# Kernel optimization log

Measured on AMD Instinct MI355X. Metric: run time of the kernel, lower is better.

The kernel has to match this reference:

```python
import jax, jax.numpy as jnp
import numpy as np

D_MODEL = 512
N_HEADS = 8
D_FF = 2048
B, L = 4, 2048
EPS = 1e-5


def _layernorm(x, g, b):
    mu = jnp.mean(x, axis=-1, keepdims=True)
    var = jnp.mean(jnp.square(x - mu), axis=-1, keepdims=True)
    return (x - mu) * jax.lax.rsqrt(var + EPS) * g + b


def setup_inputs() -> dict:
    key = jax.random.key(0)
    ks = jax.random.split(key, 8)
    s = 0.02
    return {
        'x': jax.random.normal(ks[0], (B, L, D_MODEL), jnp.float32),
        'Wq': jax.random.normal(ks[1], (D_MODEL, D_MODEL), jnp.float32) * s,
        'bq': jnp.zeros((D_MODEL,), jnp.float32),
        'Wk': jax.random.normal(ks[2], (D_MODEL, D_MODEL), jnp.float32) * s,
        'bk': jnp.zeros((D_MODEL,), jnp.float32),
        'Wv': jax.random.normal(ks[3], (D_MODEL, D_MODEL), jnp.float32) * s,
        'bv': jnp.zeros((D_MODEL,), jnp.float32),
        'Wo': jax.random.normal(ks[4], (D_MODEL, D_MODEL), jnp.float32) * s,
        'bo': jnp.zeros((D_MODEL,), jnp.float32),
        'W1': jax.random.normal(ks[5], (D_MODEL, D_FF), jnp.float32) * s,
        'b1': jnp.zeros((D_FF,), jnp.float32),
        'W2': jax.random.normal(ks[6], (D_FF, D_MODEL), jnp.float32) * s,
        'b2': jnp.zeros((D_MODEL,), jnp.float32),
        'g1': jnp.ones((D_MODEL,), jnp.float32),
        'be1': jnp.zeros((D_MODEL,), jnp.float32),
        'g2': jnp.ones((D_MODEL,), jnp.float32),
        'be2': jnp.zeros((D_MODEL,), jnp.float32),
    }


def reference(x, Wq, bq, Wk, bk, Wv, bv, Wo, bo, W1, b1, W2, b2, g1, be1, g2, be2):
    B_, L_, D = x.shape
    H = N_HEADS
    E = D // H
    q = (x @ Wq + bq).reshape(B_, L_, H, E)
    k = (x @ Wk + bk).reshape(B_, L_, H, E)
    v = (x @ Wv + bv).reshape(B_, L_, H, E)
    scale = 1.0 / jnp.sqrt(jnp.float32(E))
    # full [B,H,L,S] scores (mask_flag=False -> no causal mask)
    scores = jnp.einsum('blhe,bshe->bhls', q, k)
    A = jax.nn.softmax(scale * scores, axis=-1)
    V = jnp.einsum('bhls,bshd->blhd', A, v).reshape(B_, L_, D)
    attn_out = V @ Wo + bo
    x = _layernorm(x + attn_out, g1, be1)
    h = jax.nn.gelu(x @ W1 + b1, approximate=False)  # torch nn.GELU default = exact erf
    x = _layernorm(x + (h @ W2 + b2), g2, be2)
    return x
```

## Files before the change

### kernel.cpp

```cpp
#include <hip/hip_runtime.h>
#include <math.h>

#define DM 512
#define LSEQ 2048
#define BATCH 4
#define NH 8
#define EH 64
#define DFF 2048
#define MTOK (BATCH*LSEQ)
#define QKVW 1536
#define QSCL 0.18033688011112042f

using short8  = __attribute__((ext_vector_type(8))) short;
using floatx4 = __attribute__((ext_vector_type(4))) float;

__device__ __forceinline__ short f2b(float f) {
    unsigned u = __float_as_uint(f);
    return (short)((u + 0x7FFFu + ((u >> 16) & 1u)) >> 16);
}
__device__ __forceinline__ float b2f(short s) {
    return __uint_as_float(((unsigned)(unsigned short)s) << 16);
}
__device__ __forceinline__ void load_lds16(const short* g, short* l) {
    __builtin_amdgcn_global_load_lds(
        (const __attribute__((address_space(1))) void*)g,
        (__attribute__((address_space(3))) void*)l, 16, 0, 0);
}
#define MFMA_BF16(a, b, c) __builtin_amdgcn_mfma_f32_16x16x32_bf16(a, b, c, 0, 0, 0)

__global__ __launch_bounds__(256) void prep_kernel(
    const float* __restrict__ Wq, const float* __restrict__ Wk,
    const float* __restrict__ Wv, const float* __restrict__ Wo,
    const float* __restrict__ W1, const float* __restrict__ W2,
    const float* __restrict__ x,
    const float* __restrict__ bq, const float* __restrict__ bk,
    const float* __restrict__ bv,
    short* __restrict__ Wqkvt, short* __restrict__ Wot,
    short* __restrict__ W1t, short* __restrict__ W2t,
    short* __restrict__ xb, float* __restrict__ bqkv)
{
    __shared__ float t[64][65];
    const int bid = blockIdx.x;
    const int tid = threadIdx.x;

    if (bid >= 2880) {
        #pragma unroll
        for (int j = 0; j < 6; ++j) {
            const int i = j * 256 + tid;
            bqkv[i] = (i < 512) ? bq[i] : (i < 1024 ? bk[i - 512] : bv[i - 1024]);
        }
        return;
    }
    if (bid >= 832) {
        const long i = ((long)(bid - 832) * 256 + tid) * 8;
        float4 a = *(const float4*)(x + i);
        float4 b = *(const float4*)(x + i + 4);
        short tt[8] = { f2b(a.x), f2b(a.y), f2b(a.z), f2b(a.w),
                        f2b(b.x), f2b(b.y), f2b(b.z), f2b(b.w) };
        *(float4*)(xb + i) = *(float4*)tt;
        return;
    }
    const float* src; short* dst; int C, R, bx, by;
    if (bid < 256) {
        const int w = bid >> 6, sub = bid & 63;
        src = (w == 0) ? Wq : (w == 1) ? Wk : Wv;
        dst = Wqkvt + (long)w * 262144;
        R = 512; C = 512; bx = sub & 7; by = sub >> 3;
    } else if (bid < 320) {
        const int sub = bid - 256;
        src = Wo; dst = Wot; R = 512; C = 512; bx = sub & 7; by = sub >> 3;
    } else if (bid < 576) {
        const int sub = bid - 320;
        src = W1; dst = W1t; R = 512; C = 2048; bx = sub & 31; by = sub >> 5;
    } else {
        const int sub = bid - 576;
        src = W2; dst = W2t; R = 2048; C = 512; bx = sub & 7; by = sub >> 3;
    }
    const int r0 = by * 64, c0 = bx * 64;
    const int r = tid >> 2, cs = (tid & 3) * 16;
    const float* ip = src + (long)(r0 + r) * C + c0 + cs;
    #pragma unroll
    for (int i = 0; i < 4; ++i) {
        float4 v = *(const float4*)(ip + i * 4);
        t[r][cs + i*4 + 0] = v.x; t[r][cs + i*4 + 1] = v.y;
        t[r][cs + i*4 + 2] = v.z; t[r][cs + i*4 + 3] = v.w;
    }
    __syncthreads();
    short tmp[16];
    #pragma unroll
    for (int j = 0; j < 16; ++j) tmp[j] = f2b(t[cs + j][r]);
    short* op = dst + (long)(c0 + r) * R + r0 + cs;
    *(float4*)op       = *(float4*)&tmp[0];
    *(float4*)(op + 8) = *(float4*)&tmp[8];
}

template<int TN, int DO_GELU, int QKV>
__global__ __launch_bounds__(256, 4) void mfma_gemm(
    const short* __restrict__ A, const short* __restrict__ Bt,
    const float* __restrict__ bias, short* __restrict__ C,
    short* __restrict__ VtOut, int M, int N, int K, int lda, int ldc)
{
    constexpr int NJ = TN / 32;
    constexpr int NB = TN / 64;
    __shared__ short As[2][128][32];
    __shared__ short Bs[2][TN][32];

    const int tid  = threadIdx.x;
    const int wave = tid >> 6;
    const int lane = tid & 63;
    const int qd   = lane >> 4;
    const int sl   = lane & 15;
    const int m0 = blockIdx.y * 128;
    const int n0 = blockIdx.x * TN;
    const int wm = (wave & 1) * 64;
    const int wn = (wave >> 1) * (TN / 2);
    const int srow = lane >> 2;
    const int scol = (lane & 3) * 8;

    floatx4 acc[4][NJ];
    const floatx4 fz = {0.f, 0.f, 0.f, 0.f};
    #pragma unroll
    for (int i = 0; i < 4; ++i)
        #pragma unroll
        for (int j = 0; j < NJ; ++j) acc[i][j] = fz;

    const short* Abase = A  + (long)m0 * lda + scol;
    const short* Bbase = Bt + (long)n0 * K   + scol;

    #pragma unroll
    for (int it = 0; it < 2; ++it) {
        const int rg = wave * 2 + it;
        load_lds16(Abase + (long)(rg*16 + srow) * lda, &As[0][rg * 16][0]);
    }
    #pragma unroll
    for (int it = 0; it < NB; ++it) {
        const int rg = wave * NB + it;
        load_lds16(Bbase + (long)(rg*16 + srow) * K, &Bs[0][rg * 16][0]);
    }

    const int NIT = K / 32;
    for (int kit = 0; kit < NIT; ++kit) {
        const int cur = kit & 1;
        __syncthreads();
        if (kit + 1 < NIT) {
            const int nk = (kit + 1) * 32;
            #pragma unroll
            for (int it = 0; it < 2; ++it) {
                const int rg = wave * 2 + it;
                load_lds16(Abase + (long)(rg*16 + srow) * lda + nk, &As[1 - cur][rg * 16][0]);
            }
            #pragma unroll
            for (int it = 0; it < NB; ++it) {
                const int rg = wave * NB + it;
                load_lds16(Bbase + (long)(rg*16 + srow) * K + nk, &Bs[1 - cur][rg * 16][0]);
            }
        }
        short8 af[4], bf[NJ];
        #pragma unroll
        for (int t = 0; t < 4; ++t)
            af[t] = *(const short8*)&As[cur][wm + t*16 + sl][qd * 8];
        #pragma unroll
        for (int t = 0; t < NJ; ++t)
            bf[t] = *(const short8*)&Bs[cur][wn + t*16 + sl][qd * 8];
        #pragma unroll
        for (int i = 0; i < 4; ++i)
            #pragma unroll
            for (int j = 0; j < NJ; ++j)
                acc[i][j] = MFMA_BF16(af[i], bf[j], acc[i][j]);
    }

    #pragma unroll
    for (int j = 0; j < NJ; ++j) {
        const int col = n0 + wn + j*16 + sl;
        const float bv = bias[col];
        #pragma unroll
        for (int i = 0; i < 4; ++i) {
            #pragma unroll
            for (int r = 0; r < 4; ++r) {
                const int row = m0 + wm + i*16 + qd*4 + r;
                float v = acc[i][j][r] + bv;
                if (DO_GELU) v = 0.5f * v * (1.0f + erff(v * 0.70710678118654752f));
                if (QKV) {
                    if (col < 512) v *= QSCL;
                    const short bb = f2b(v);
                    if (col < 1024) {
                        C[(long)row * 1024 + col] = bb;
                    } else {
                        const int e = col - 1024;
                        const int b_ = row >> 11, l = row & 2047;
                        VtOut[(((long)(b_*8 + (e >> 6))) * 64 + (e & 63)) * 2048 + l] = bb;
                    }
                } else {
                    C[(long)row * ldc + col] = f2b(v);
                }
            }
        }
    }
}

__global__ __launch_bounds__(256, 3) void mfma_attn(
    const short* __restrict__ QK, const short* __restrict__ VtG,
    short* __restrict__ O)
{
    __shared__ short Ks[2][2][64][32];
    __shared__ short Vs[2][2][64][32];
    __shared__ short Ps[4][32][72];

    const int tid  = threadIdx.x;
    const int wave = tid >> 6;
    const int lane = tid & 63;
    const int qd   = lane >> 4;
    const int sl   = lane & 15;
    const int srow = lane >> 2;
    const int scol = (lane & 3) * 8;

    const int bid = blockIdx.x;
    const int h  = bid & 7;
    const int b  = (bid >> 3) & 3;
    const int qt = bid >> 5;
    const int tok0 = b * LSEQ;
    const int q0 = qt * 128;
    const short* Kbase = QK + (long)tok0 * 1024 + 512 + h * EH
                         + (long)(wave*16 + srow) * 1024 + scol;
    const short* Vbase = VtG + ((long)(b * NH + h)) * EH * 2048
                         + (long)(wave*16 + srow) * 2048 + scol;

    {
        const int lr = tid >> 1;
        const int lc = (tid & 1) * 32;
        const short* qp = QK + (long)(tok0 + q0 + lr) * 1024 + h * EH + lc;
        short* dp = &Ps[wave][lr & 31][lc];
        *(float4*)(dp)      = *(const float4*)(qp);
        *(float4*)(dp + 8)  = *(const float4*)(qp + 8);
        *(float4*)(dp + 16) = *(const float4*)(qp + 16);
        *(float4*)(dp + 24) = *(const float4*)(qp + 24);
    }
    short8 aq[2][2];
    #pragma unroll
    for (int q2 = 0; q2 < 2; ++q2)
        #pragma unroll
        for (int ks = 0; ks < 2; ++ks)
            aq[q2][ks] = *(const short8*)&Ps[wave][q2*16 + sl][ks*32 + qd*8];

    float l_i[2][4] = {};
    floatx4 oacc[2][4];
    const floatx4 fz = {0.f, 0.f, 0.f, 0.f};
    #pragma unroll
    for (int q2 = 0; q2 < 2; ++q2)
        #pragma unroll
        for (int t = 0; t < 4; ++t) oacc[q2][t] = fz;

    #pragma unroll
    for (int p = 0; p < 2; ++p) {
        load_lds16(Kbase + p*32,            &Ks[0][p][wave*16][0]);
        load_lds16(Vbase + p*32,            &Vs[0][p][wave*16][0]);
    }

    for (int kt = 0; kt < 32; ++kt) {
        const int cur = kt & 1;
        __syncthreads();
        if (kt + 1 < 32) {
            #pragma unroll
            for (int p = 0; p < 2; ++p) {
                load_lds16(Kbase + (long)(kt+1)*64*1024 + p*32, &Ks[1 - cur][p][wave*16][0]);
                load_lds16(Vbase + (kt+1)*64 + p*32,            &Vs[1 - cur][p][wave*16][0]);
            }
        }

        floatx4 s[2][4];
        #pragma unroll
        for (int q2 = 0; q2 < 2; ++q2)
            #pragma unroll
            for (int t = 0; t < 4; ++t) s[q2][t] = fz;
        #pragma unroll
        for (int ks = 0; ks < 2; ++ks)
            #pragma unroll
            for (int t = 0; t < 4; ++t) {
                short8 bk = *(const short8*)&Ks[cur][ks][t*16 + sl][qd * 8];
                s[0][t] = MFMA_BF16(aq[0][ks], bk, s[0][t]);
                s[1][t] = MFMA_BF16(aq[1][ks], bk, s[1][t]);
            }

        #pragma unroll
        for (int q2 = 0; q2 < 2; ++q2)
            #pragma unroll
            for (int t = 0; t < 4; ++t) {
                const int pg = (((t*2 + (sl >> 3)) ^ qd) << 3) | (sl & 7);
                #pragma unroll
                for (int r = 0; r < 4; ++r) {
                    const float pv = __builtin_amdgcn_exp2f(s[q2][t][r]);
                    l_i[q2][r] += pv;
                    Ps[wave][q2*16 + qd*4 + r][pg] = (short)(__float_as_uint(pv) >> 16);
                }
            }

        #pragma unroll
        for (int ks = 0; ks < 2; ++ks) {
            const int pgr = ((ks*4 + qd) ^ ((sl >> 2) & 3)) * 8;
            short8 ap0 = *(const short8*)&Ps[wave][sl][pgr];
            short8 ap1 = *(const short8*)&Ps[wave][16 + sl][pgr];
            #pragma unroll
            for (int t = 0; t < 4; ++t) {
                short8 bv = *(const short8*)&Vs[cur][ks][t*16 + sl][qd * 8];
                oacc[0][t] = MFMA_BF16(ap0, bv, oacc[0][t]);
                oacc[1][t] = MFMA_BF16(ap1, bv, oacc[1][t]);
            }
        }
    }

    float linv[2][4];
    #pragma unroll
    for (int q2 = 0; q2 < 2; ++q2)
        #pragma unroll
        for (int r = 0; r < 4; ++r) {
            float l = l_i[q2][r];
            l += __shfl_xor(l, 1);
            l += __shfl_xor(l, 2);
            l += __shfl_xor(l, 4);
            l += __shfl_xor(l, 8);
            linv[q2][r] = 1.0f / l;
        }
    #pragma unroll
    for (int q2 = 0; q2 < 2; ++q2)
        #pragma unroll
        for (int t = 0; t < 4; ++t)
            #pragma unroll
            for (int r = 0; r < 4; ++r) {
                const int row = tok0 + q0 + wave*32 + q2*16 + qd*4 + r;
                const int col = h * EH + t*16 + sl;
                O[(long)row * DM + col] = f2b(oacc[q2][t][r] * linv[q2][r]);
            }
}

template<int X_BF16, int OUT_F32>
__global__ __launch_bounds__(256) void add_ln_kernel(
    const void* __restrict__ Xv, const short* __restrict__ R,
    const float* __restrict__ g, const float* __restrict__ beta,
    void* __restrict__ outv)
{
    const int row = blockIdx.x;
    const int tid = threadIdx.x;
    float x0, x1;
    if (X_BF16) {
        const short* xp = (const short*)Xv + (long)row * DM;
        x0 = b2f(xp[tid]); x1 = b2f(xp[tid + 256]);
    } else {
        const float* xp = (const float*)Xv + (long)row * DM;
        x0 = xp[tid]; x1 = xp[tid + 256];
    }
    const short* rp = R + (long)row * DM;
    const float v0 = x0 + b2f(rp[tid]);
    const float v1 = x1 + b2f(rp[tid + 256]);
    float s = v0 + v1, sq = v0*v0 + v1*v1;
    #pragma unroll
    for (int o = 32; o > 0; o >>= 1) {
        s  += __shfl_down(s, o);
        sq += __shfl_down(sq, o);
    }
    __shared__ float ss[4], ssq[4];
    const int wid = tid >> 6, lane = tid & 63;
    if (lane == 0) { ss[wid] = s; ssq[wid] = sq; }
    __syncthreads();
    const float S  = ss[0] + ss[1] + ss[2] + ss[3];
    const float SQ = ssq[0] + ssq[1] + ssq[2] + ssq[3];
    const float mean = S * (1.0f / DM);
    const float var  = SQ * (1.0f / DM) - mean * mean;
    const float rstd = rsqrtf(var + 1e-5f);
    const float o0 = (v0 - mean) * rstd * g[tid] + beta[tid];
    const float o1 = (v1 - mean) * rstd * g[tid + 256] + beta[tid + 256];
    if (OUT_F32) {
        float* op = (float*)outv + (long)row * DM;
        op[tid] = o0; op[tid + 256] = o1;
    } else {
        short* op = (short*)outv + (long)row * DM;
        op[tid] = f2b(o0); op[tid + 256] = f2b(o1);
    }
}

extern "C" void kernel_launch(void* const* d_in, const int* in_sizes, int n_in,
                              void* d_out, int out_size, void* d_ws, size_t ws_size,
                              hipStream_t stream)
{
    const float* x   = (const float*)d_in[0];
    const float* Wq  = (const float*)d_in[1];
    const float* bq  = (const float*)d_in[2];
    const float* Wk  = (const float*)d_in[3];
    const float* bk  = (const float*)d_in[4];
    const float* Wv  = (const float*)d_in[5];
    const float* bv  = (const float*)d_in[6];
    const float* Wo  = (const float*)d_in[7];
    const float* bo  = (const float*)d_in[8];
    const float* W1  = (const float*)d_in[9];
    const float* b1  = (const float*)d_in[10];
    const float* W2  = (const float*)d_in[11];
    const float* b2  = (const float*)d_in[12];
    const float* g1  = (const float*)d_in[13];
    const float* be1 = (const float*)d_in[14];
    const float* g2  = (const float*)d_in[15];
    const float* be2 = (const float*)d_in[16];
    float* out = (float*)d_out;

    short* ws    = (short*)d_ws;
    short* Wqkvt = ws;
    short* Wot   = Wqkvt + 786432;
    short* W1t   = Wot + 262144;
    short* W2t   = W1t + 1048576;
    float* bqkv  = (float*)(W2t + 1048576);
    short* xb    = (short*)(bqkv + 1536);
    short* qk    = xb + 4194304;
    short* VtG   = qk + 8388608;
    short* Ob    = VtG + 4194304;
    short* res   = Ob + 4194304;
    short* hbuf  = qk;

    const dim3 blk(256);

    prep_kernel<<<dim3(2881), blk, 0, stream>>>(
        Wq, Wk, Wv, Wo, W1, W2, x, bq, bk, bv,
        Wqkvt, Wot, W1t, W2t, xb, bqkv);

    mfma_gemm<128, 0, 1><<<dim3(12, 64), blk, 0, stream>>>(
        xb, Wqkvt, bqkv, qk, VtG, MTOK, QKVW, DM, DM, 0);

    mfma_attn<<<dim3(512), blk, 0, stream>>>(qk, VtG, Ob);

    mfma_gemm<64, 0, 0><<<dim3(8, 64), blk, 0, stream>>>(
        Ob, Wot, bo, res, nullptr, MTOK, DM, DM, DM, DM);

    add_ln_kernel<0, 0><<<dim3(MTOK), blk, 0, stream>>>(x, res, g1, be1, xb);

    mfma_gemm<128, 1, 0><<<dim3(16, 64), blk, 0, stream>>>(
        xb, W1t, b1, hbuf, nullptr, MTOK, DFF, DM, DM, DFF);

    mfma_gemm<64, 0, 0><<<dim3(8, 64), blk, 0, stream>>>(
        hbuf, W2t, b2, res, nullptr, MTOK, DM, DFF, DFF, DM);

    add_ln_kernel<1, 1><<<dim3(MTOK), blk, 0, stream>>>(xb, res, g2, be2, out);
}
```

Measured before the change: 289.8 us.

## Halve attention query tile, compute transposed scores, use tanh GELU, vector V stores

The attention kernel now gives each wave 16 query rows instead of 32 and launches twice as many blocks. It computes S^T by swapping the MFMA operands so each lane packs four probabilities into one 8-byte LDS write, and the row sum is reduced with fewer shuffles. The GEMM epilogue swaps exact erf GELU for a tanh approximation built on exp2/rcp, and writes the transposed V output as packed 4-element stores using round-half-up bf16 packing. The intent is more parallelism and fewer scalar stores and transcendental ops, at the cost of reloading K/V tiles twice as often per query and a small deviation from exact GELU.

```diff
diff --git a/kernel.cpp b/kernel.cpp
--- a/kernel.cpp
+++ b/kernel.cpp
@@ -20,6 +20,17 @@
 }
 __device__ __forceinline__ float b2f(short s) {
     return __uint_as_float(((unsigned)(unsigned short)s) << 16);
+}
+__device__ __forceinline__ unsigned pack2bf(float lo, float hi) {
+    return __builtin_amdgcn_perm(__float_as_uint(hi) + 0x8000u,
+                                 __float_as_uint(lo) + 0x8000u, 0x07060302u);
+}
+__device__ __forceinline__ float gelu_tanh(float v) {
+    float v2 = v * v;
+    float y  = v * fmaf(0.0356774081f, v2, 0.7978845608f);
+    float e  = __builtin_amdgcn_exp2f(y * 2.885390082f);
+    float r  = __builtin_amdgcn_rcpf(e + 1.0f);
+    return v * (1.0f - r);
 }
 __device__ __forceinline__ void load_lds16(const short* g, short* l) {
     __builtin_amdgcn_global_load_lds(
@@ -172,27 +183,35 @@
     #pragma unroll
     for (int j = 0; j < NJ; ++j) {
         const int col = n0 + wn + j*16 + sl;
-        const float bv = bias[col];
+        const float bvs = bias[col];
         #pragma unroll
         for (int i = 0; i < 4; ++i) {
+            float v[4];
             #pragma unroll
             for (int r = 0; r < 4; ++r) {
-                const int row = m0 + wm + i*16 + qd*4 + r;
-                float v = acc[i][j][r] + bv;
-                if (DO_GELU) v = 0.5f * v * (1.0f + erff(v * 0.70710678118654752f));
-                if (QKV) {
-                    if (col < 512) v *= QSCL;
-                    const short bb = f2b(v);
-                    if (col < 1024) {
-                        C[(long)row * 1024 + col] = bb;
-                    } else {
-                        const int e = col - 1024;
-                        const int b_ = row >> 11, l = row & 2047;
-                        VtOut[(((long)(b_*8 + (e >> 6))) * 64 + (e & 63)) * 2048 + l] = bb;
-                    }
+                float tv = acc[i][j][r] + bvs;
+                if (DO_GELU) tv = gelu_tanh(tv);
+                v[r] = tv;
+            }
+            const int row0 = m0 + wm + i*16 + qd*4;
+            if (QKV) {
+                if (col < 1024) {
+                    const float s = (col < 512) ? QSCL : 1.0f;
+                    #pragma unroll
+                    for (int r = 0; r < 4; ++r)
+                        C[(long)(row0 + r) * 1024 + col] = f2b(v[r] * s);
                 } else {
-                    C[(long)row * ldc + col] = f2b(v);
+                    const int e = col - 1024;
+                    const int b_ = row0 >> 11, l0 = row0 & 2047;
+                    uint2 w;
+                    w.x = pack2bf(v[0], v[1]);
+                    w.y = pack2bf(v[2], v[3]);
+                    *(uint2*)&VtOut[(((long)(b_*8 + (e >> 6))) * 64 + (e & 63)) * 2048 + l0] = w;
                 }
+            } else {
+                #pragma unroll
+                for (int r = 0; r < 4; ++r)
+                    C[(long)(row0 + r) * ldc + col] = f2b(v[r]);
             }
         }
     }
@@ -204,7 +223,7 @@
 {
     __shared__ short Ks[2][2][64][32];
     __shared__ short Vs[2][2][64][32];
-    __shared__ short Ps[4][32][72];
+    __shared__ short PT[4][16][72];
 
     const int tid  = threadIdx.x;
     const int wave = tid >> 6;
@@ -219,41 +238,36 @@
     const int b  = (bid >> 3) & 3;
     const int qt = bid >> 5;
     const int tok0 = b * LSEQ;
-    const int q0 = qt * 128;
+    const int q0 = qt * 64;
+
     const short* Kbase = QK + (long)tok0 * 1024 + 512 + h * EH
                          + (long)(wave*16 + srow) * 1024 + scol;
     const short* Vbase = VtG + ((long)(b * NH + h)) * EH * 2048
                          + (long)(wave*16 + srow) * 2048 + scol;
 
     {
-        const int lr = tid >> 1;
-        const int lc = (tid & 1) * 32;
-        const short* qp = QK + (long)(tok0 + q0 + lr) * 1024 + h * EH + lc;
-        short* dp = &Ps[wave][lr & 31][lc];
-        *(float4*)(dp)      = *(const float4*)(qp);
-        *(float4*)(dp + 8)  = *(const float4*)(qp + 8);
-        *(float4*)(dp + 16) = *(const float4*)(qp + 16);
-        *(float4*)(dp + 24) = *(const float4*)(qp + 24);
-    }
-    short8 aq[2][2];
-    #pragma unroll
-    for (int q2 = 0; q2 < 2; ++q2)
-        #pragma unroll
-        for (int ks = 0; ks < 2; ++ks)
-            aq[q2][ks] = *(const short8*)&Ps[wave][q2*16 + sl][ks*32 + qd*8];
-
-    float l_i[2][4] = {};
-    floatx4 oacc[2][4];
+        const int qr = lane >> 2;
+        const int qc = (lane & 3) * 16;
+        const short* qp = QK + (long)(tok0 + q0 + wave*16 + qr) * 1024 + h * EH + qc;
+        short* dp = &PT[wave][qr][qc];
+        *(float4*)dp       = *(const float4*)qp;
+        *(float4*)(dp + 8) = *(const float4*)(qp + 8);
+    }
+    short8 aq[2];
+    #pragma unroll
+    for (int ks = 0; ks < 2; ++ks)
+        aq[ks] = *(const short8*)&PT[wave][sl][ks*32 + qd*8];
+
+    float l_i = 0.f;
+    floatx4 oacc[4];
     const floatx4 fz = {0.f, 0.f, 0.f, 0.f};
     #pragma unroll
-    for (int q2 = 0; q2 < 2; ++q2)
-        #pragma unroll
-        for (int t = 0; t < 4; ++t) oacc[q2][t] = fz;
+    for (int t = 0; t < 4; ++t) oacc[t] = fz;
 
     #pragma unroll
     for (int p = 0; p < 2; ++p) {
-        load_lds16(Kbase + p*32,            &Ks[0][p][wave*16][0]);
-        load_lds16(Vbase + p*32,            &Vs[0][p][wave*16][0]);
+        load_lds16(Kbase + p*32, &Ks[0][p][wave*16][0]);
+        load_lds16(Vbase + p*32, &Vs[0][p][wave*16][0]);
     }
 
     for (int kt = 0; kt < 32; ++kt) {
@@ -267,69 +281,56 @@
             }
         }
 
-        floatx4 s[2][4];
-        #pragma unroll
-        for (int q2 = 0; q2 < 2; ++q2)
-            #pragma unroll
-            for (int t = 0; t < 4; ++t) s[q2][t] = fz;
+        floatx4 sT[4];
+        #pragma unroll
+        for (int t = 0; t < 4; ++t) sT[t] = fz;
         #pragma unroll
         for (int ks = 0; ks < 2; ++ks)
             #pragma unroll
             for (int t = 0; t < 4; ++t) {
-                short8 bk = *(const short8*)&Ks[cur][ks][t*16 + sl][qd * 8];
-                s[0][t] = MFMA_BF16(aq[0][ks], bk, s[0][t]);
-                s[1][t] = MFMA_BF16(aq[1][ks], bk, s[1][t]);
-            }
-
-        #pragma unroll
-        for (int q2 = 0; q2 < 2; ++q2)
-            #pragma unroll
-            for (int t = 0; t < 4; ++t) {
-                const int pg = (((t*2 + (sl >> 3)) ^ qd) << 3) | (sl & 7);
-                #pragma unroll
-                for (int r = 0; r < 4; ++r) {
-                    const float pv = __builtin_amdgcn_exp2f(s[q2][t][r]);
-                    l_i[q2][r] += pv;
-                    Ps[wave][q2*16 + qd*4 + r][pg] = (short)(__float_as_uint(pv) >> 16);
-                }
-            }
+                short8 ak = *(const short8*)&Ks[cur][ks][t*16 + sl][qd * 8];
+                sT[t] = MFMA_BF16(ak, aq[ks], sT[t]);
+            }
+
+        #pragma unroll
+        for (int t = 0; t < 4; ++t) {
+            const float p0 = __builtin_amdgcn_exp2f(sT[t][0]);
+            const float p1 = __builtin_amdgcn_exp2f(sT[t][1]);
+            const float p2 = __builtin_amdgcn_exp2f(sT[t][2]);
+            const float p3 = __builtin_amdgcn_exp2f(sT[t][3]);
+            l_i += (p0 + p1) + (p2 + p3);
+            uint2 w;
+            w.x = pack2bf(p0, p1);
+            w.y = pack2bf(p2, p3);
+            *(uint2*)&PT[wave][sl][t*16 + qd*4] = w;
+        }
 
         #pragma unroll
         for (int ks = 0; ks < 2; ++ks) {
-            const int pgr = ((ks*4 + qd) ^ ((sl >> 2) & 3)) * 8;
-            short8 ap0 = *(const short8*)&Ps[wave][sl][pgr];
-            short8 ap1 = *(const short8*)&Ps[wave][16 + sl][pgr];
+            short8 ap = *(const short8*)&PT[wave][sl][ks*32 + qd*8];
             #pragma unroll
             for (int t = 0; t < 4; ++t) {
                 short8 bv = *(const short8*)&Vs[cur][ks][t*16 + sl][qd * 8];
-                oacc[0][t] = MFMA_BF16(ap0, bv, oacc[0][t]);
-                oacc[1][t] = MFMA_BF16(ap1, bv, oacc[1][t]);
-            }
-        }
-    }
-
-    float linv[2][4];
-    #pragma unroll
-    for (int q2 = 0; q2 < 2; ++q2)
+                oacc[t] = MFMA_BF16(ap, bv, oacc[t]);
+            }
+        }
+    }
+
+    l_i += __shfl_xor(l_i, 16);
+    l_i += __shfl_xor(l_i, 32);
+    float linv[4];
+    #pragma unroll
+    for (int r = 0; r < 4; ++r)
+        linv[r] = 1.0f / __shfl(l_i, qd*4 + r, 64);
+
+    #pragma unroll
+    for (int t = 0; t < 4; ++t)
         #pragma unroll
         for (int r = 0; r < 4; ++r) {
-            float l = l_i[q2][r];
-            l += __shfl_xor(l, 1);
-            l += __shfl_xor(l, 2);
-            l += __shfl_xor(l, 4);
-            l += __shfl_xor(l, 8);
-            linv[q2][r] = 1.0f / l;
-        }
-    #pragma unroll
-    for (int q2 = 0; q2 < 2; ++q2)
-        #pragma unroll
-        for (int t = 0; t < 4; ++t)
-            #pragma unroll
-            for (int r = 0; r < 4; ++r) {
-                const int row = tok0 + q0 + wave*32 + q2*16 + qd*4 + r;
-                const int col = h * EH + t*16 + sl;
-                O[(long)row * DM + col] = f2b(oacc[q2][t][r] * linv[q2][r]);
-            }
+            const int row = tok0 + q0 + wave*16 + qd*4 + r;
+            const int col = h * EH + t*16 + sl;
+            O[(long)row * DM + col] = f2b(oacc[t][r] * linv[r]);
+        }
 }
 
 template<int X_BF16, int OUT_F32>
@@ -422,7 +423,7 @@
     mfma_gemm<128, 0, 1><<<dim3(12, 64), blk, 0, stream>>>(
         xb, Wqkvt, bqkv, qk, VtG, MTOK, QKVW, DM, DM, 0);
 
-    mfma_attn<<<dim3(512), blk, 0, stream>>>(qk, VtG, Ob);
+    mfma_attn<<<dim3(1024), blk, 0, stream>>>(qk, VtG, Ob);
 
     mfma_gemm<64, 0, 0><<<dim3(8, 64), blk, 0, stream>>>(
         Ob, Wot, bo, res, nullptr, MTOK, DM, DM, DM, DM);
```

New measurement: 291.3 us. Within noise of the previous version (+0.5%).
